# Performance work log

Measured on AMD Instinct MI355X. Metric: run time of the kernel, lower is better.

The kernel has to match this reference:

```python
import jax, jax.numpy as jnp
import numpy as np

N, H, S = 100, 16, 6  # n_subactors, neurons, state_size
B, T = 128, 128


def setup_inputs() -> dict:
    key = jax.random.key(0)
    ks = jax.random.split(key, 12)
    sc = 1.0 / np.sqrt(H)
    inp = {
        "x":   jax.random.normal(ks[0], (B, T, N, S), dtype=jnp.float32),
        # stacked per-subactor GRU weights (torch gate order: r, z, n)
        "Wih": jax.random.uniform(ks[1], (N, 3 * H, S), minval=-sc, maxval=sc, dtype=jnp.float32),
        "Whh": jax.random.uniform(ks[2], (N, 3 * H, H), minval=-sc, maxval=sc, dtype=jnp.float32),
        "bih": jax.random.uniform(ks[3], (N, 3 * H), minval=-sc, maxval=sc, dtype=jnp.float32),
        "bhh": jax.random.uniform(ks[4], (N, 3 * H), minval=-sc, maxval=sc, dtype=jnp.float32),
        # stacked per-subactor MLP weights
        "W1": jax.random.uniform(ks[5], (N, H, H), minval=-sc, maxval=sc, dtype=jnp.float32),
        "b1": jax.random.uniform(ks[6], (N, H), minval=-sc, maxval=sc, dtype=jnp.float32),
        "W2": jax.random.uniform(ks[7], (N, H, H), minval=-sc, maxval=sc, dtype=jnp.float32),
        "b2": jax.random.uniform(ks[8], (N, H), minval=-sc, maxval=sc, dtype=jnp.float32),
        "W3": jax.random.uniform(ks[9], (N, 1, H), minval=-sc, maxval=sc, dtype=jnp.float32),
        "b3": jax.random.uniform(ks[10], (N, 1), minval=-sc, maxval=sc, dtype=jnp.float32),
    }
    return inp


def reference(x, Wih, Whh, bih, bhh, W1, b1, W2, b2, W3, b3):
    b, t, n, s = x.shape
    h = Whh.shape[-1]
    # input projections for all timesteps/subactors at once: [B,T,N,3H]
    xi = jnp.einsum('btns,ngs->btng', x, Wih) + bih

    def step(hprev, xt):  # hprev [B,N,H], xt [B,N,3H]
        hh = jnp.einsum('bnh,ngh->bng', hprev, Whh) + bhh
        xr, xz, xn = jnp.split(xt, 3, axis=-1)
        hr, hz, hn = jnp.split(hh, 3, axis=-1)
        r = jax.nn.sigmoid(xr + hr)
        z = jax.nn.sigmoid(xz + hz)
        nn_ = jnp.tanh(xn + r * hn)
        hnew = (1.0 - z) * nn_ + z * hprev
        return hnew, hnew

    h0 = jnp.zeros((b, n, h), dtype=x.dtype)
    _, hs = jax.lax.scan(step, h0, jnp.moveaxis(xi, 1, 0))  # [T,B,N,H]
    hs = jnp.moveaxis(hs, 0, 1)  # [B,T,N,H]

    y = jax.nn.relu(jnp.einsum('btnh,nkh->btnk', hs, W1) + b1)
    y = jax.nn.relu(jnp.einsum('btnh,nkh->btnk', y, W2) + b2)
    y = jax.nn.relu(jnp.einsum('btnh,nkh->btnk', y, W3) + b3)  # [B,T,N,1]
    # torch: stack over subactors -> [N,B,T,1] then .view(-1, t, nzones)
    return jnp.transpose(y, (2, 0, 1, 3)).reshape(-1, t, n)
```

## Files before the change

kernel.cpp:

```cpp
#include <hip/hip_runtime.h>

namespace {

constexpr int kN = 100;
constexpr int kH = 16;
constexpr int kS = 6;
constexpr int kB = 128;
constexpr int kT = 128;
constexpr int kNS = kN * kS;
constexpr int kXB = kT * kNS;

typedef float f32x4 __attribute__((ext_vector_type(4)));
typedef short bf16x8 __attribute__((ext_vector_type(8)));

union Frag {
  unsigned u[4];
  bf16x8 v;
};

__device__ __forceinline__ unsigned pkbf(float a, float b) {
  unsigned ua = __builtin_bit_cast(unsigned, a);
  unsigned ub = __builtin_bit_cast(unsigned, b);
  ua += 0x7fffu + ((ua >> 16) & 1u);
  ub += 0x7fffu + ((ub >> 16) & 1u);
  return (ua >> 16) | (ub & 0xffff0000u);
}

__device__ __forceinline__ float rcp_fast(float v) {
  return __builtin_amdgcn_rcpf(v);
}
__device__ __forceinline__ float sigm(float v) {
  return rcp_fast(1.0f + __expf(-v));
}
__device__ __forceinline__ float tanh_fast(float v) {
  return 1.0f - 2.0f * rcp_fast(1.0f + __expf(2.0f * v));
}

__device__ __forceinline__ f32x4 mfma16(bf16x8 a, bf16x8 b, f32x4 c) {
  return __builtin_amdgcn_mfma_f32_16x16x32_bf16(a, b, c, 0, 0, 0);
}

__device__ __forceinline__ void mkA(Frag& F, int qt, const float* hrow,
                                    const float* xrow) {
  F.u[0] = F.u[1] = F.u[2] = F.u[3] = 0u;
  if (hrow) {
    F.u[0] = pkbf(hrow[4 * qt + 0], hrow[4 * qt + 1]);
    F.u[1] = pkbf(hrow[4 * qt + 2], hrow[4 * qt + 3]);
  }
  if (xrow && qt < 3) {
    F.u[2] = pkbf(xrow[2 * qt + 0], xrow[2 * qt + 1]);
  }
}

}

__global__ __launch_bounds__(64) void actor_local(
    const float* __restrict__ x, const float* __restrict__ Wih,
    const float* __restrict__ Whh, const float* __restrict__ bih,
    const float* __restrict__ bhh, const float* __restrict__ W1,
    const float* __restrict__ b1, const float* __restrict__ W2,
    const float* __restrict__ b2, const float* __restrict__ W3,
    const float* __restrict__ b3, float* __restrict__ out) {
  const int tid = (int)threadIdx.x;
  const int j = tid & 15;
  const int qt = tid >> 4;
  const int n = (int)blockIdx.x >> 3;
  const int bt = (int)blockIdx.x & 7;

  Frag Ar, Az, Anh, Anx, Ay1, Ay2;
  mkA(Ar, qt, Whh + ((size_t)n * 48 + j) * 16, Wih + ((size_t)n * 48 + j) * 6);
  mkA(Az, qt, Whh + ((size_t)n * 48 + 16 + j) * 16,
      Wih + ((size_t)n * 48 + 16 + j) * 6);
  mkA(Anh, qt, Whh + ((size_t)n * 48 + 32 + j) * 16, nullptr);
  mkA(Anx, qt, nullptr, Wih + ((size_t)n * 48 + 32 + j) * 6);
  mkA(Ay1, qt, W1 + ((size_t)n * 16 + j) * 16, nullptr);
  mkA(Ay2, qt, W2 + ((size_t)n * 16 + j) * 16, nullptr);

  float br_[4], bz_[4], bin_[4], bhn_[4], b1e[4], b2e[4], w3r[4];
#pragma unroll
  for (int r = 0; r < 4; ++r) {
    const int gi = n * 48 + 4 * qt + r;
    br_[r] = bih[gi] + bhh[gi];
    bz_[r] = bih[gi + 16] + bhh[gi + 16];
    bin_[r] = bih[gi + 32];
    bhn_[r] = bhh[gi + 32];
    const int hi = n * 16 + 4 * qt + r;
    b1e[r] = b1[hi];
    b2e[r] = b2[hi];
    w3r[r] = W3[hi];
  }
  const float b3s = b3[n];

  const int b = bt * 16 + j;
  const float* px = x + (size_t)b * kXB + (size_t)n * kS + (qt < 3 ? 2 * qt : 0);
  float* outp = out + ((size_t)n * kB + b) * kT;

  const f32x4 zero4 = {0.f, 0.f, 0.f, 0.f};

  float2 xr[2];
  xr[0] = *(const float2*)(px + 0 * kNS);
  xr[1] = *(const float2*)(px + 1 * kNS);

  float hprev[4] = {0.f, 0.f, 0.f, 0.f};
  unsigned P0 = 0u, P1 = 0u;

  auto doY = [&](const f32x4& Cy1, int tout) {
    float y1v[4];
#pragma unroll
    for (int r = 0; r < 4; ++r) y1v[r] = fmaxf(Cy1[r] + b1e[r], 0.f);
    Frag By;
    By.u[0] = pkbf(y1v[0], y1v[1]);
    By.u[1] = pkbf(y1v[2], y1v[3]);
    By.u[2] = 0u;
    By.u[3] = 0u;
    const f32x4 Cy2 = mfma16(Ay2.v, By.v, zero4);
    float s = 0.f;
#pragma unroll
    for (int r = 0; r < 4; ++r) s += fmaxf(Cy2[r] + b2e[r], 0.f) * w3r[r];
    s += __shfl_xor(s, 16);
    s += __shfl_xor(s, 32);
    const float y3 = fmaxf(s + b3s, 0.f);
    if (tout >= 0 && qt == 0) outp[tout] = y3;
  };

  for (int t2 = 0; t2 < kT; t2 += 2) {
#pragma unroll
    for (int k = 0; k < 2; ++k) {
      const int t = t2 + k;
      Frag Bf;
      Bf.u[0] = P0;
      Bf.u[1] = P1;
      Bf.u[2] = (qt < 3) ? pkbf(xr[k].x, xr[k].y) : 0u;
      Bf.u[3] = 0u;

      {
        int tc = t + 2;
        if (tc > kT - 1) tc = kT - 1;
        xr[k] = *(const float2*)(px + (size_t)tc * kNS);
      }

      const f32x4 Cr = mfma16(Ar.v, Bf.v, zero4);
      const f32x4 Cz = mfma16(Az.v, Bf.v, zero4);
      const f32x4 Chn = mfma16(Anh.v, Bf.v, zero4);
      const f32x4 Cxn = mfma16(Anx.v, Bf.v, zero4);
      const f32x4 Cy1 = mfma16(Ay1.v, Bf.v, zero4);

      doY(Cy1, t - 1);

#pragma unroll
      for (int r = 0; r < 4; ++r) {
        const float rr = sigm(Cr[r] + br_[r]);
        const float zz = sigm(Cz[r] + bz_[r]);
        const float nn =
            tanh_fast((Cxn[r] + bin_[r]) + rr * (Chn[r] + bhn_[r]));
        hprev[r] = nn + zz * (hprev[r] - nn);
      }
      P0 = pkbf(hprev[0], hprev[1]);
      P1 = pkbf(hprev[2], hprev[3]);
    }
  }

  {
    Frag Bf;
    Bf.u[0] = P0;
    Bf.u[1] = P1;
    Bf.u[2] = 0u;
    Bf.u[3] = 0u;
    const f32x4 Cy1 = mfma16(Ay1.v, Bf.v, zero4);
    doY(Cy1, kT - 1);
  }
}

extern "C" void kernel_launch(void* const* d_in, const int* in_sizes, int n_in,
                              void* d_out, int out_size, void* d_ws,
                              size_t ws_size, hipStream_t stream) {
  const float* x = (const float*)d_in[0];
  const float* Wih = (const float*)d_in[1];
  const float* Whh = (const float*)d_in[2];
  const float* bih = (const float*)d_in[3];
  const float* bhh = (const float*)d_in[4];
  const float* W1 = (const float*)d_in[5];
  const float* b1 = (const float*)d_in[6];
  const float* W2 = (const float*)d_in[7];
  const float* b2 = (const float*)d_in[8];
  const float* W3 = (const float*)d_in[9];
  const float* b3 = (const float*)d_in[10];
  float* out = (float*)d_out;

  actor_local<<<dim3(kN * 8), dim3(64), 0, stream>>>(x, Wih, Whh, bih, bhh, W1,
                                                     b1, W2, b2, W3, b3, out);
}
```

Baseline: 158.6 us.

## Software-pipeline MLP head across timesteps and fold biases and log2e into MFMA

```diff
diff --git a/kernel.cpp b/kernel.cpp
--- a/kernel.cpp
+++ b/kernel.cpp
@@ -9,6 +9,7 @@
 constexpr int kT = 128;
 constexpr int kNS = kN * kS;
 constexpr int kXB = kT * kNS;
+constexpr float kL2E = 1.44269504088896340736f;
 
 typedef float f32x4 __attribute__((ext_vector_type(4)));
 typedef short bf16x8 __attribute__((ext_vector_type(8)));
@@ -29,11 +30,8 @@
 __device__ __forceinline__ float rcp_fast(float v) {
   return __builtin_amdgcn_rcpf(v);
 }
-__device__ __forceinline__ float sigm(float v) {
-  return rcp_fast(1.0f + __expf(-v));
-}
-__device__ __forceinline__ float tanh_fast(float v) {
-  return 1.0f - 2.0f * rcp_fast(1.0f + __expf(2.0f * v));
+__device__ __forceinline__ float exp2_fast(float v) {
+  return __builtin_amdgcn_exp2f(v);
 }
 
 __device__ __forceinline__ f32x4 mfma16(bf16x8 a, bf16x8 b, f32x4 c) {
@@ -41,20 +39,20 @@
 }
 
 __device__ __forceinline__ void mkA(Frag& F, int qt, const float* hrow,
-                                    const float* xrow) {
+                                    const float* xrow, float sc) {
   F.u[0] = F.u[1] = F.u[2] = F.u[3] = 0u;
   if (hrow) {
-    F.u[0] = pkbf(hrow[4 * qt + 0], hrow[4 * qt + 1]);
-    F.u[1] = pkbf(hrow[4 * qt + 2], hrow[4 * qt + 3]);
+    F.u[0] = pkbf(hrow[4 * qt + 0] * sc, hrow[4 * qt + 1] * sc);
+    F.u[1] = pkbf(hrow[4 * qt + 2] * sc, hrow[4 * qt + 3] * sc);
   }
   if (xrow && qt < 3) {
-    F.u[2] = pkbf(xrow[2 * qt + 0], xrow[2 * qt + 1]);
-  }
-}
-
-}
-
-__global__ __launch_bounds__(64) void actor_local(
+    F.u[2] = pkbf(xrow[2 * qt + 0] * sc, xrow[2 * qt + 1] * sc);
+  }
+}
+
+}
+
+__global__ __launch_bounds__(64) void actor_pipe(
     const float* __restrict__ x, const float* __restrict__ Wih,
     const float* __restrict__ Whh, const float* __restrict__ bih,
     const float* __restrict__ bhh, const float* __restrict__ W1,
@@ -68,34 +66,35 @@
   const int bt = (int)blockIdx.x & 7;
 
   Frag Ar, Az, Anh, Anx, Ay1, Ay2;
-  mkA(Ar, qt, Whh + ((size_t)n * 48 + j) * 16, Wih + ((size_t)n * 48 + j) * 6);
+  mkA(Ar, qt, Whh + ((size_t)n * 48 + j) * 16, Wih + ((size_t)n * 48 + j) * 6,
+      kL2E);
   mkA(Az, qt, Whh + ((size_t)n * 48 + 16 + j) * 16,
-      Wih + ((size_t)n * 48 + 16 + j) * 6);
-  mkA(Anh, qt, Whh + ((size_t)n * 48 + 32 + j) * 16, nullptr);
-  mkA(Anx, qt, nullptr, Wih + ((size_t)n * 48 + 32 + j) * 6);
-  mkA(Ay1, qt, W1 + ((size_t)n * 16 + j) * 16, nullptr);
-  mkA(Ay2, qt, W2 + ((size_t)n * 16 + j) * 16, nullptr);
-
-  float br_[4], bz_[4], bin_[4], bhn_[4], b1e[4], b2e[4], w3r[4];
+      Wih + ((size_t)n * 48 + 16 + j) * 6, kL2E);
+  mkA(Anh, qt, Whh + ((size_t)n * 48 + 32 + j) * 16, nullptr, 2.0f * kL2E);
+  mkA(Anx, qt, nullptr, Wih + ((size_t)n * 48 + 32 + j) * 6, 2.0f * kL2E);
+  mkA(Ay1, qt, W1 + ((size_t)n * 16 + j) * 16, nullptr, 1.0f);
+  mkA(Ay2, qt, W2 + ((size_t)n * 16 + j) * 16, nullptr, 1.0f);
+
+  f32x4 Cbr, Cbz, Cbhn, Cbin, Cb1, Cb2;
+  float w3r[4];
 #pragma unroll
   for (int r = 0; r < 4; ++r) {
     const int gi = n * 48 + 4 * qt + r;
-    br_[r] = bih[gi] + bhh[gi];
-    bz_[r] = bih[gi + 16] + bhh[gi + 16];
-    bin_[r] = bih[gi + 32];
-    bhn_[r] = bhh[gi + 32];
+    Cbr[r] = (bih[gi] + bhh[gi]) * kL2E;
+    Cbz[r] = (bih[gi + 16] + bhh[gi + 16]) * kL2E;
+    Cbin[r] = bih[gi + 32] * 2.0f * kL2E;
+    Cbhn[r] = bhh[gi + 32] * 2.0f * kL2E;
     const int hi = n * 16 + 4 * qt + r;
-    b1e[r] = b1[hi];
-    b2e[r] = b2[hi];
+    Cb1[r] = b1[hi];
+    Cb2[r] = b2[hi];
     w3r[r] = W3[hi];
   }
   const float b3s = b3[n];
 
   const int b = bt * 16 + j;
-  const float* px = x + (size_t)b * kXB + (size_t)n * kS + (qt < 3 ? 2 * qt : 0);
+  const float* px =
+      x + (size_t)b * kXB + (size_t)n * kS + (qt < 3 ? 2 * qt : 0);
   float* outp = out + ((size_t)n * kB + b) * kT;
-
-  const f32x4 zero4 = {0.f, 0.f, 0.f, 0.f};
 
   float2 xr[2];
   xr[0] = *(const float2*)(px + 0 * kNS);
@@ -104,71 +103,99 @@
   float hprev[4] = {0.f, 0.f, 0.f, 0.f};
   unsigned P0 = 0u, P1 = 0u;
 
-  auto doY = [&](const f32x4& Cy1, int tout) {
-    float y1v[4];
-#pragma unroll
-    for (int r = 0; r < 4; ++r) y1v[r] = fmaxf(Cy1[r] + b1e[r], 0.f);
-    Frag By;
-    By.u[0] = pkbf(y1v[0], y1v[1]);
-    By.u[1] = pkbf(y1v[2], y1v[3]);
-    By.u[2] = 0u;
-    By.u[3] = 0u;
-    const f32x4 Cy2 = mfma16(Ay2.v, By.v, zero4);
-    float s = 0.f;
-#pragma unroll
-    for (int r = 0; r < 4; ++r) s += fmaxf(Cy2[r] + b2e[r], 0.f) * w3r[r];
-    s += __shfl_xor(s, 16);
-    s += __shfl_xor(s, 32);
-    const float y3 = fmaxf(s + b3s, 0.f);
-    if (tout >= 0 && qt == 0) outp[tout] = y3;
-  };
-
-  for (int t2 = 0; t2 < kT; t2 += 2) {
-#pragma unroll
-    for (int k = 0; k < 2; ++k) {
-      const int t = t2 + k;
+  const f32x4 zero4 = {0.f, 0.f, 0.f, 0.f};
+  f32x4 Cy1p = zero4;
+  f32x4 Cy2p = zero4;
+  float s4[4] = {0.f, 0.f, 0.f, 0.f};
+
+  auto step = [&](int t, bool doRec, bool doA, bool doB, bool doC) {
+    f32x4 Cr, Cz, Chn, Cxn, Cy1n = Cy1p;
+    if (t <= kT) {
+      const int sl = t & 1;
       Frag Bf;
       Bf.u[0] = P0;
       Bf.u[1] = P1;
-      Bf.u[2] = (qt < 3) ? pkbf(xr[k].x, xr[k].y) : 0u;
+      Bf.u[2] = (qt < 3) ? pkbf(xr[sl].x, xr[sl].y) : 0u;
       Bf.u[3] = 0u;
-
       {
         int tc = t + 2;
         if (tc > kT - 1) tc = kT - 1;
-        xr[k] = *(const float2*)(px + (size_t)tc * kNS);
-      }
-
-      const f32x4 Cr = mfma16(Ar.v, Bf.v, zero4);
-      const f32x4 Cz = mfma16(Az.v, Bf.v, zero4);
-      const f32x4 Chn = mfma16(Anh.v, Bf.v, zero4);
-      const f32x4 Cxn = mfma16(Anx.v, Bf.v, zero4);
-      const f32x4 Cy1 = mfma16(Ay1.v, Bf.v, zero4);
-
-      doY(Cy1, t - 1);
-
+        xr[sl] = *(const float2*)(px + (size_t)tc * kNS);
+      }
+      if (doRec) {
+        Cr = mfma16(Ar.v, Bf.v, Cbr);
+        Cz = mfma16(Az.v, Bf.v, Cbz);
+        Chn = mfma16(Anh.v, Bf.v, Cbhn);
+        Cxn = mfma16(Anx.v, Bf.v, Cbin);
+      }
+      Cy1n = mfma16(Ay1.v, Bf.v, Cb1);
+    }
+
+    if (doB) {
+      float s = fmaxf(Cy2p[0], 0.f) * w3r[0];
+      s += fmaxf(Cy2p[1], 0.f) * w3r[1];
+      s += fmaxf(Cy2p[2], 0.f) * w3r[2];
+      s += fmaxf(Cy2p[3], 0.f) * w3r[3];
+      s4[(t - 3) & 3] = s;
+    }
+
+    if (doA) {
+      Frag By;
+      By.u[0] = pkbf(fmaxf(Cy1p[0], 0.f), fmaxf(Cy1p[1], 0.f));
+      By.u[1] = pkbf(fmaxf(Cy1p[2], 0.f), fmaxf(Cy1p[3], 0.f));
+      By.u[2] = 0u;
+      By.u[3] = 0u;
+      Cy2p = mfma16(Ay2.v, By.v, Cb2);
+    }
+
+    if (doC) {
+      float v0 = s4[0], v1 = s4[1], v2 = s4[2], v3 = s4[3];
+      v0 += __shfl_xor(v0, 16);
+      v1 += __shfl_xor(v1, 16);
+      v2 += __shfl_xor(v2, 16);
+      v3 += __shfl_xor(v3, 16);
+      v0 += __shfl_xor(v0, 32);
+      v1 += __shfl_xor(v1, 32);
+      v2 += __shfl_xor(v2, 32);
+      v3 += __shfl_xor(v3, 32);
+      if (qt == 0) {
+        float4 o = {fmaxf(v0 + b3s, 0.f), fmaxf(v1 + b3s, 0.f),
+                    fmaxf(v2 + b3s, 0.f), fmaxf(v3 + b3s, 0.f)};
+        *(float4*)(outp + (t - 6)) = o;
+      }
+    }
+
+    if (doRec) {
 #pragma unroll
       for (int r = 0; r < 4; ++r) {
-        const float rr = sigm(Cr[r] + br_[r]);
-        const float zz = sigm(Cz[r] + bz_[r]);
-        const float nn =
-            tanh_fast((Cxn[r] + bin_[r]) + rr * (Chn[r] + bhn_[r]));
+        const float rr = rcp_fast(1.f + exp2_fast(-Cr[r]));
+        const float zz = rcp_fast(1.f + exp2_fast(-Cz[r]));
+        const float np = Cxn[r] + rr * Chn[r];
+        const float nn = 1.f - 2.f * rcp_fast(1.f + exp2_fast(np));
         hprev[r] = nn + zz * (hprev[r] - nn);
       }
       P0 = pkbf(hprev[0], hprev[1]);
       P1 = pkbf(hprev[2], hprev[3]);
     }
-  }
-
-  {
-    Frag Bf;
-    Bf.u[0] = P0;
-    Bf.u[1] = P1;
-    Bf.u[2] = 0u;
-    Bf.u[3] = 0u;
-    const f32x4 Cy1 = mfma16(Ay1.v, Bf.v, zero4);
-    doY(Cy1, kT - 1);
-  }
+
+    Cy1p = Cy1n;
+  };
+
+  step(0, true, false, false, false);
+  step(1, true, false, false, false);
+  step(2, true, true, false, false);
+  step(3, true, true, true, false);
+
+  for (int t4 = 4; t4 < kT; t4 += 4) {
+    step(t4 + 0, true, true, true, false);
+    step(t4 + 1, true, true, true, false);
+    step(t4 + 2, true, true, true, true);
+    step(t4 + 3, true, true, true, false);
+  }
+
+  step(kT, false, true, true, false);
+  step(kT + 1, false, true, true, false);
+  step(kT + 2, false, false, true, true);
 }
 
 extern "C" void kernel_launch(void* const* d_in, const int* in_sizes, int n_in,
@@ -187,6 +214,6 @@
   const float* b3 = (const float*)d_in[10];
   float* out = (float*)d_out;
 
-  actor_local<<<dim3(kN * 8), dim3(64), 0, stream>>>(x, Wih, Whh, bih, bhh, W1,
-                                                     b1, W2, b2, W3, b3, out);
-}
+  actor_pipe<<<dim3(kN * 8), dim3(64), 0, stream>>>(x, Wih, Whh, bih, bhh, W1,
+                                                    b1, W2, b2, W3, b3, out);
+}
```

Result: faster. 143.9 us (-9.2%).
